# Optimization experiments

Hardware: AMD Instinct MI355X
Metric: run time of the kernel (lower is better)

The kernel has to match this reference:

```python
import jax, jax.numpy as jnp
import numpy as np

DIM = 1024
HID = 2048
E = 4

def setup_inputs() -> dict:
    key = jax.random.key(0)
    ks = jax.random.split(key, 7)
    s = lambda fan_in: 1.0 / np.sqrt(fan_in)
    x = jax.random.normal(ks[0], (2, 2048, DIM), dtype=jnp.float32)
    W1 = jax.random.uniform(ks[1], (E, DIM, HID), jnp.float32, -s(DIM), s(DIM))
    b1 = jax.random.uniform(ks[2], (E, HID), jnp.float32, -s(DIM), s(DIM))
    W2 = jax.random.uniform(ks[3], (E, HID, DIM), jnp.float32, -s(HID), s(HID))
    b2 = jax.random.uniform(ks[4], (E, DIM), jnp.float32, -s(HID), s(HID))
    Wr = jax.random.uniform(ks[5], (DIM, E), jnp.float32, -s(DIM), s(DIM))
    br = jax.random.uniform(ks[6], (E,), jnp.float32, -s(DIM), s(DIM))
    return {"x": x, "W1": W1, "b1": b1, "W2": W2, "b2": b2, "Wr": Wr, "br": br}

def reference(x, W1, b1, W2, b2, Wr, br):
    # router softmax weights: [B,T,E]
    weights = jax.nn.softmax(x @ Wr + br, axis=-1)
    # all-expert MLP: hidden [B,T,E,H]
    h = jax.nn.gelu(jnp.einsum('btd,edh->bteh', x, W1) + b1, approximate=False)
    # expert outputs [B,T,E,D]
    y = jnp.einsum('bteh,ehd->bted', h, W2) + b2
    # softmax-weighted combine over experts
    return jnp.einsum('bte,bted->btd', weights, y)
```

## Files before the change

### kernel.cpp

```cpp
#include <hip/hip_runtime.h>
#include <hip/hip_bf16.h>
#include <math.h>

#define DIM 1024
#define HID 2048
#define NE  4
#define NT  4096
#define KW  (NE*HID)
#define KSPLIT 2
#define KCH (KW / KSPLIT)

typedef __attribute__((ext_vector_type(8))) short short8;
typedef __attribute__((ext_vector_type(4))) short short4v;
typedef __attribute__((ext_vector_type(4))) float floatx4;


__device__ __forceinline__ void async_cp16(const void* g, void* l) {
  __builtin_amdgcn_global_load_lds(
      (const __attribute__((address_space(1))) void*)g,
      (__attribute__((address_space(3))) void*)l, 16, 0, 0);
}

__device__ __forceinline__ short f2bf(float f) {
  union { float f; unsigned u; } x; x.f = f;
  unsigned r = x.u + 0x7fffu + ((x.u >> 16) & 1u);
  return (short)(r >> 16);
}

__device__ __forceinline__ float gelu_fast(float v) {
  float u = 1.595769122f * (v + 0.044715f * v * v * v);
  return v * __builtin_amdgcn_rcpf(1.0f + __expf(-u));
}

__global__ void router_cvt(const float* __restrict__ x, const float* __restrict__ Wr,
                           const float* __restrict__ br, float* __restrict__ wgt,
                           short* __restrict__ xb) {
  const int wv = threadIdx.x >> 6, lane = threadIdx.x & 63;
  const int t = blockIdx.x * 4 + wv;
  const float* xr = x + (size_t)t * DIM;
  short* xo = xb + (size_t)t * DIM;
  float a0 = 0.f, a1 = 0.f, a2 = 0.f, a3 = 0.f;
  #pragma unroll
  for (int p = 0; p < 4; p++) {
    const int d = p * 256 + lane * 4;
    floatx4 v = *(const floatx4*)&xr[d];
    short4v o;
    #pragma unroll
    for (int j = 0; j < 4; j++) {
      o[j] = f2bf(v[j]);
      floatx4 wr = *(const floatx4*)&Wr[(d + j) * 4];
      a0 += v[j] * wr[0]; a1 += v[j] * wr[1];
      a2 += v[j] * wr[2]; a3 += v[j] * wr[3];
    }
    *(short4v*)&xo[d] = o;
  }
  #pragma unroll
  for (int off = 32; off; off >>= 1) {
    a0 += __shfl_down(a0, off);
    a1 += __shfl_down(a1, off);
    a2 += __shfl_down(a2, off);
    a3 += __shfl_down(a3, off);
  }
  a0 = __shfl(a0, 0); a1 = __shfl(a1, 0); a2 = __shfl(a2, 0); a3 = __shfl(a3, 0);
  float s0 = a0 + br[0], s1 = a1 + br[1], s2 = a2 + br[2], s3 = a3 + br[3];
  float m = fmaxf(fmaxf(s0, s1), fmaxf(s2, s3));
  float e0 = __expf(s0 - m), e1 = __expf(s1 - m), e2 = __expf(s2 - m), e3 = __expf(s3 - m);
  float inv = 1.f / (e0 + e1 + e2 + e3);
  float v = (lane == 0) ? e0 : (lane == 1) ? e1 : (lane == 2) ? e2 : e3;
  if (lane < 4) wgt[t * 4 + lane] = v * inv;
}

#define TP_PADR 136
__global__ void transpose_all(const float* __restrict__ W1, short* __restrict__ w1t,
                              const float* __restrict__ W2, short* __restrict__ w2t) {
  __shared__ __align__(16) short tile[32 * TP_PADR];
  const int b = blockIdx.x;
  const float* in; short* out; int R, C, xt, yt;
  if (b < 2048) {
    const int e = b >> 9, rem = b & 511;
    xt = rem & 63; yt = rem >> 6; R = DIM; C = HID;
    in = W1 + (size_t)e * DIM * HID; out = w1t + (size_t)e * DIM * HID;
  } else {
    const int rem = b - 2048;
    xt = rem & 31; yt = rem >> 5; R = KW; C = DIM;
    in = W2; out = w2t;
  }
  const int c0 = xt * 32, r0 = yt * 128;
  const int t = threadIdx.x;
  const int cin = (t & 7) * 4;
  const int rin = t >> 3;
  #pragma unroll
  for (int i = 0; i < 4; i++) {
    const int r = rin + i * 32;
    floatx4 v = *(const floatx4*)&in[(size_t)(r0 + r) * C + c0 + cin];
    #pragma unroll
    for (int j = 0; j < 4; j++)
      tile[(cin + j) * TP_PADR + r] = f2bf(v[j]);
  }
  __syncthreads();
  const int ct = t >> 3;
  #pragma unroll
  for (int i = 0; i < 2; i++) {
    const int rc = (t & 7) + 8 * i;
    short8 vv = *(const short8*)&tile[ct * TP_PADR + rc * 8];
    *(short8*)&out[(size_t)(c0 + ct) * R + r0 + rc * 8] = vv;
  }
}


__global__ __launch_bounds__(256, 2)
void gemm1_kernel(const short* __restrict__ xb, const short* __restrict__ w1t,
                  const float* __restrict__ b1, const float* __restrict__ wgt,
                  short* __restrict__ hw) {
  const int b = blockIdx.x;
  const int xcd = b & 7, slot = b >> 3;
  const int m_grp = xcd & 3, e_pair = xcd >> 1 & 2;
  const int n_idx = slot & 15, m_off = (slot >> 4) & 7, e_off = slot >> 7;
  const int e  = (xcd >> 2) * 2 + e_off;
  const int m0 = (m_grp * 8 + m_off) * 128;
  const int n0 = n_idx * 128;
  (void)e_pair;
  const int tid = threadIdx.x;
  const int lane = tid & 63;
  const int wv = tid >> 6;
  const int wm = (wv >> 1) * 64, wn = (wv & 1) * 64;
  const int quad = lane >> 4, lrow = lane & 15;
  const int sr  = tid >> 3;
  const int kof = ((tid & 7) ^ (sr & 7)) * 8;
  const int rkey = lrow & 7;

  __shared__ __align__(16) short As[128 * 64];
  __shared__ __align__(16) short Bs[128 * 64];

  const short* Ap = xb;
  const short* Bp = w1t + (size_t)e * HID * DIM;

  floatx4 acc[4][4];
  #pragma unroll
  for (int i = 0; i < 4; i++)
    #pragma unroll
    for (int j = 0; j < 4; j++) acc[i][j] = (floatx4)0.f;

  for (int k0 = 0; k0 < DIM; k0 += 64) {
    __syncthreads();
    #pragma unroll
    for (int c = 0; c < 4; c++)
      async_cp16(Ap + (size_t)(m0 + c * 32 + sr) * DIM + k0 + kof,
                 As + (c * 256 + tid) * 8);
    #pragma unroll
    for (int c = 0; c < 4; c++)
      async_cp16(Bp + (size_t)(n0 + c * 32 + sr) * DIM + k0 + kof,
                 Bs + (c * 256 + tid) * 8);
    __syncthreads();
    #pragma unroll
    for (int kk = 0; kk < 2; kk++) {
      short8 af[4], bf[4];
      const int ko = ((kk * 4 + quad) ^ rkey) * 8;
      #pragma unroll
      for (int i = 0; i < 4; i++)
        af[i] = *(const short8*)&As[(wm + i * 16 + lrow) * 64 + ko];
      #pragma unroll
      for (int j = 0; j < 4; j++)
        bf[j] = *(const short8*)&Bs[(wn + j * 16 + lrow) * 64 + ko];
      #pragma unroll
      for (int i = 0; i < 4; i++)
        #pragma unroll
        for (int j = 0; j < 4; j++)
          acc[i][j] = __builtin_amdgcn_mfma_f32_16x16x32_bf16(af[i], bf[j], acc[i][j], 0, 0, 0);
    }
  }

  #pragma unroll
  for (int i = 0; i < 4; i++) {
    const int rbase = m0 + wm + i * 16 + quad * 4;
    float wv4[4];
    #pragma unroll
    for (int r = 0; r < 4; r++) wv4[r] = wgt[(rbase + r) * NE + e];
    #pragma unroll
    for (int j = 0; j < 4; j++) {
      const int col = n0 + wn + j * 16 + lrow;
      const float b1v = b1[e * HID + col];
      #pragma unroll
      for (int r = 0; r < 4; r++) {
        float v = acc[i][j][r] + b1v;
        hw[(size_t)(rbase + r) * KW + e * HID + col] = f2bf(wv4[r] * gelu_fast(v));
      }
    }
  }
}

__global__ __launch_bounds__(256, 2)
void gemm2_kernel(const short* __restrict__ hw, const short* __restrict__ w2t,
                  const float* __restrict__ b2, const float* __restrict__ wgt,
                  float* __restrict__ out, float* __restrict__ part) {
  const int b = blockIdx.x;
  const int xcd = b & 7, slot = b >> 3;
  const int m_grp = xcd & 3, kz = xcd >> 2;
  const int n_idx = slot & 7, m_off = slot >> 3;
  const int m0 = (m_grp * 8 + m_off) * 128;
  const int n0 = n_idx * 128;
  const int tid = threadIdx.x;
  const int lane = tid & 63;
  const int wv = tid >> 6;
  const int wm = (wv >> 1) * 64, wn = (wv & 1) * 64;
  const int quad = lane >> 4, lrow = lane & 15;
  const int sr  = tid >> 3;
  const int kof = ((tid & 7) ^ (sr & 7)) * 8;
  const int rkey = lrow & 7;

  __shared__ __align__(16) short As[128 * 64];
  __shared__ __align__(16) short Bs[128 * 64];

  floatx4 acc[4][4];
  #pragma unroll
  for (int i = 0; i < 4; i++)
    #pragma unroll
    for (int j = 0; j < 4; j++) acc[i][j] = (floatx4)0.f;

  const int kbeg = kz * KCH;
  for (int kk0 = 0; kk0 < KCH; kk0 += 64) {
    const int k0 = kbeg + kk0;
    __syncthreads();
    #pragma unroll
    for (int c = 0; c < 4; c++)
      async_cp16(hw + (size_t)(m0 + c * 32 + sr) * KW + k0 + kof,
                 As + (c * 256 + tid) * 8);
    #pragma unroll
    for (int c = 0; c < 4; c++)
      async_cp16(w2t + (size_t)(n0 + c * 32 + sr) * KW + k0 + kof,
                 Bs + (c * 256 + tid) * 8);
    __syncthreads();
    #pragma unroll
    for (int kk = 0; kk < 2; kk++) {
      short8 af[4], bf[4];
      const int ko = ((kk * 4 + quad) ^ rkey) * 8;
      #pragma unroll
      for (int i = 0; i < 4; i++)
        af[i] = *(const short8*)&As[(wm + i * 16 + lrow) * 64 + ko];
      #pragma unroll
      for (int j = 0; j < 4; j++)
        bf[j] = *(const short8*)&Bs[(wn + j * 16 + lrow) * 64 + ko];
      #pragma unroll
      for (int i = 0; i < 4; i++)
        #pragma unroll
        for (int j = 0; j < 4; j++)
          acc[i][j] = __builtin_amdgcn_mfma_f32_16x16x32_bf16(af[i], bf[j], acc[i][j], 0, 0, 0);
    }
  }

  if (kz == 0) {
    #pragma unroll
    for (int i = 0; i < 4; i++) {
      const int rbase = m0 + wm + i * 16 + quad * 4;
      floatx4 wr[4];
      #pragma unroll
      for (int r = 0; r < 4; r++) wr[r] = *(const floatx4*)&wgt[(rbase + r) * NE];
      #pragma unroll
      for (int j = 0; j < 4; j++) {
        const int col = n0 + wn + j * 16 + lrow;
        float b2v[4];
        #pragma unroll
        for (int eI = 0; eI < 4; eI++) b2v[eI] = b2[eI * DIM + col];
        #pragma unroll
        for (int r = 0; r < 4; r++) {
          float bias = wr[r][0] * b2v[0] + wr[r][1] * b2v[1] +
                       wr[r][2] * b2v[2] + wr[r][3] * b2v[3];
          out[(size_t)(rbase + r) * DIM + col] = acc[i][j][r] + bias;
        }
      }
    }
  } else {
    #pragma unroll
    for (int i = 0; i < 4; i++) {
      const int rbase = m0 + wm + i * 16 + quad * 4;
      #pragma unroll
      for (int j = 0; j < 4; j++) {
        const int col = n0 + wn + j * 16 + lrow;
        #pragma unroll
        for (int r = 0; r < 4; r++)
          part[(size_t)(rbase + r) * DIM + col] = acc[i][j][r];
      }
    }
  }
}

__global__ void reduce_out(float* __restrict__ out, const float* __restrict__ part) {
  int i = (blockIdx.x * 256 + threadIdx.x) * 4;
  floatx4 v = *(const floatx4*)&out[i];
  floatx4 a = *(const floatx4*)&part[i];
  v = v + a;
  *(floatx4*)&out[i] = v;
}


extern "C" void kernel_launch(void* const* d_in, const int* in_sizes, int n_in,
                              void* d_out, int out_size, void* d_ws, size_t ws_size,
                              hipStream_t stream) {
  const float* x  = (const float*)d_in[0];
  const float* W1 = (const float*)d_in[1];
  const float* b1 = (const float*)d_in[2];
  const float* W2 = (const float*)d_in[3];
  const float* b2 = (const float*)d_in[4];
  const float* Wr = (const float*)d_in[5];
  const float* br = (const float*)d_in[6];
  float* out = (float*)d_out;

  char* ws = (char*)d_ws;
  float* wgt = (float*)(ws);
  short* w2t = (short*)(ws + 65536);
  short* hw  = (short*)(ws + 65536 + 16777216);
  short* xb  = (short*)(ws + 65536 + 16777216 + 67108864);
  short* w1t = (short*)(ws + 65536 + 16777216 + 67108864 + 8388608);
  float* part= (float*)(ws + 65536 + 16777216 + 67108864);

  hipLaunchKernelGGL(router_cvt, dim3(NT / 4), dim3(256), 0, stream, x, Wr, br, wgt, xb);
  hipLaunchKernelGGL(transpose_all, dim3(2048 + 2048), dim3(256), 0, stream,
                     W1, w1t, W2, w2t);
  hipLaunchKernelGGL(gemm1_kernel, dim3(2048), dim3(256), 0, stream,
                     xb, w1t, b1, wgt, hw);
  hipLaunchKernelGGL(gemm2_kernel, dim3(512), dim3(256), 0, stream,
                     hw, w2t, b2, wgt, out, part);
  hipLaunchKernelGGL(reduce_out, dim3(NT * DIM / 1024), dim3(256), 0, stream, out, part);
}
```

Baseline: 284.1 us.

## Load B operands directly into registers, merge prep kernels, remap XCD tiling

```diff
diff --git a/kernel.cpp b/kernel.cpp
--- a/kernel.cpp
+++ b/kernel.cpp
@@ -32,49 +32,51 @@
   return v * __builtin_amdgcn_rcpf(1.0f + __expf(-u));
 }
 
-__global__ void router_cvt(const float* __restrict__ x, const float* __restrict__ Wr,
-                           const float* __restrict__ br, float* __restrict__ wgt,
-                           short* __restrict__ xb) {
-  const int wv = threadIdx.x >> 6, lane = threadIdx.x & 63;
-  const int t = blockIdx.x * 4 + wv;
-  const float* xr = x + (size_t)t * DIM;
-  short* xo = xb + (size_t)t * DIM;
-  float a0 = 0.f, a1 = 0.f, a2 = 0.f, a3 = 0.f;
-  #pragma unroll
-  for (int p = 0; p < 4; p++) {
-    const int d = p * 256 + lane * 4;
-    floatx4 v = *(const floatx4*)&xr[d];
-    short4v o;
-    #pragma unroll
-    for (int j = 0; j < 4; j++) {
-      o[j] = f2bf(v[j]);
-      floatx4 wr = *(const floatx4*)&Wr[(d + j) * 4];
-      a0 += v[j] * wr[0]; a1 += v[j] * wr[1];
-      a2 += v[j] * wr[2]; a3 += v[j] * wr[3];
-    }
-    *(short4v*)&xo[d] = o;
-  }
-  #pragma unroll
-  for (int off = 32; off; off >>= 1) {
-    a0 += __shfl_down(a0, off);
-    a1 += __shfl_down(a1, off);
-    a2 += __shfl_down(a2, off);
-    a3 += __shfl_down(a3, off);
-  }
-  a0 = __shfl(a0, 0); a1 = __shfl(a1, 0); a2 = __shfl(a2, 0); a3 = __shfl(a3, 0);
-  float s0 = a0 + br[0], s1 = a1 + br[1], s2 = a2 + br[2], s3 = a3 + br[3];
-  float m = fmaxf(fmaxf(s0, s1), fmaxf(s2, s3));
-  float e0 = __expf(s0 - m), e1 = __expf(s1 - m), e2 = __expf(s2 - m), e3 = __expf(s3 - m);
-  float inv = 1.f / (e0 + e1 + e2 + e3);
-  float v = (lane == 0) ? e0 : (lane == 1) ? e1 : (lane == 2) ? e2 : e3;
-  if (lane < 4) wgt[t * 4 + lane] = v * inv;
-}
-
 #define TP_PADR 136
-__global__ void transpose_all(const float* __restrict__ W1, short* __restrict__ w1t,
-                              const float* __restrict__ W2, short* __restrict__ w2t) {
+__global__ void prep_kernel(const float* __restrict__ x, const float* __restrict__ Wr,
+                            const float* __restrict__ br, float* __restrict__ wgt,
+                            short* __restrict__ xb,
+                            const float* __restrict__ W1, short* __restrict__ w1t,
+                            const float* __restrict__ W2, short* __restrict__ w2t) {
   __shared__ __align__(16) short tile[32 * TP_PADR];
-  const int b = blockIdx.x;
+  const int bb = blockIdx.x;
+  if (bb < 1024) {
+    const int wv = threadIdx.x >> 6, lane = threadIdx.x & 63;
+    const int t = bb * 4 + wv;
+    const float* xr = x + (size_t)t * DIM;
+    short* xo = xb + (size_t)t * DIM;
+    float a0 = 0.f, a1 = 0.f, a2 = 0.f, a3 = 0.f;
+    #pragma unroll
+    for (int p = 0; p < 4; p++) {
+      const int d = p * 256 + lane * 4;
+      floatx4 v = *(const floatx4*)&xr[d];
+      short4v o;
+      #pragma unroll
+      for (int j = 0; j < 4; j++) {
+        o[j] = f2bf(v[j]);
+        floatx4 wr = *(const floatx4*)&Wr[(d + j) * 4];
+        a0 += v[j] * wr[0]; a1 += v[j] * wr[1];
+        a2 += v[j] * wr[2]; a3 += v[j] * wr[3];
+      }
+      *(short4v*)&xo[d] = o;
+    }
+    #pragma unroll
+    for (int off = 32; off; off >>= 1) {
+      a0 += __shfl_down(a0, off);
+      a1 += __shfl_down(a1, off);
+      a2 += __shfl_down(a2, off);
+      a3 += __shfl_down(a3, off);
+    }
+    a0 = __shfl(a0, 0); a1 = __shfl(a1, 0); a2 = __shfl(a2, 0); a3 = __shfl(a3, 0);
+    float s0 = a0 + br[0], s1 = a1 + br[1], s2 = a2 + br[2], s3 = a3 + br[3];
+    float m = fmaxf(fmaxf(s0, s1), fmaxf(s2, s3));
+    float e0 = __expf(s0 - m), e1 = __expf(s1 - m), e2 = __expf(s2 - m), e3 = __expf(s3 - m);
+    float inv = 1.f / (e0 + e1 + e2 + e3);
+    float v = (lane == 0) ? e0 : (lane == 1) ? e1 : (lane == 2) ? e2 : e3;
+    if (lane < 4) wgt[t * 4 + lane] = v * inv;
+    return;
+  }
+  const int b = bb - 1024;
   const float* in; short* out; int R, C, xt, yt;
   if (b < 2048) {
     const int e = b >> 9, rem = b & 511;
@@ -114,90 +116,9 @@
                   short* __restrict__ hw) {
   const int b = blockIdx.x;
   const int xcd = b & 7, slot = b >> 3;
-  const int m_grp = xcd & 3, e_pair = xcd >> 1 & 2;
-  const int n_idx = slot & 15, m_off = (slot >> 4) & 7, e_off = slot >> 7;
-  const int e  = (xcd >> 2) * 2 + e_off;
-  const int m0 = (m_grp * 8 + m_off) * 128;
-  const int n0 = n_idx * 128;
-  (void)e_pair;
-  const int tid = threadIdx.x;
-  const int lane = tid & 63;
-  const int wv = tid >> 6;
-  const int wm = (wv >> 1) * 64, wn = (wv & 1) * 64;
-  const int quad = lane >> 4, lrow = lane & 15;
-  const int sr  = tid >> 3;
-  const int kof = ((tid & 7) ^ (sr & 7)) * 8;
-  const int rkey = lrow & 7;
-
-  __shared__ __align__(16) short As[128 * 64];
-  __shared__ __align__(16) short Bs[128 * 64];
-
-  const short* Ap = xb;
-  const short* Bp = w1t + (size_t)e * HID * DIM;
-
-  floatx4 acc[4][4];
-  #pragma unroll
-  for (int i = 0; i < 4; i++)
-    #pragma unroll
-    for (int j = 0; j < 4; j++) acc[i][j] = (floatx4)0.f;
-
-  for (int k0 = 0; k0 < DIM; k0 += 64) {
-    __syncthreads();
-    #pragma unroll
-    for (int c = 0; c < 4; c++)
-      async_cp16(Ap + (size_t)(m0 + c * 32 + sr) * DIM + k0 + kof,
-                 As + (c * 256 + tid) * 8);
-    #pragma unroll
-    for (int c = 0; c < 4; c++)
-      async_cp16(Bp + (size_t)(n0 + c * 32 + sr) * DIM + k0 + kof,
-                 Bs + (c * 256 + tid) * 8);
-    __syncthreads();
-    #pragma unroll
-    for (int kk = 0; kk < 2; kk++) {
-      short8 af[4], bf[4];
-      const int ko = ((kk * 4 + quad) ^ rkey) * 8;
-      #pragma unroll
-      for (int i = 0; i < 4; i++)
-        af[i] = *(const short8*)&As[(wm + i * 16 + lrow) * 64 + ko];
-      #pragma unroll
-      for (int j = 0; j < 4; j++)
-        bf[j] = *(const short8*)&Bs[(wn + j * 16 + lrow) * 64 + ko];
-      #pragma unroll
-      for (int i = 0; i < 4; i++)
-        #pragma unroll
-        for (int j = 0; j < 4; j++)
-          acc[i][j] = __builtin_amdgcn_mfma_f32_16x16x32_bf16(af[i], bf[j], acc[i][j], 0, 0, 0);
-    }
-  }
-
-  #pragma unroll
-  for (int i = 0; i < 4; i++) {
-    const int rbase = m0 + wm + i * 16 + quad * 4;
-    float wv4[4];
-    #pragma unroll
-    for (int r = 0; r < 4; r++) wv4[r] = wgt[(rbase + r) * NE + e];
-    #pragma unroll
-    for (int j = 0; j < 4; j++) {
-      const int col = n0 + wn + j * 16 + lrow;
-      const float b1v = b1[e * HID + col];
-      #pragma unroll
-      for (int r = 0; r < 4; r++) {
-        float v = acc[i][j][r] + b1v;
-        hw[(size_t)(rbase + r) * KW + e * HID + col] = f2bf(wv4[r] * gelu_fast(v));
-      }
-    }
-  }
-}
-
-__global__ __launch_bounds__(256, 2)
-void gemm2_kernel(const short* __restrict__ hw, const short* __restrict__ w2t,
-                  const float* __restrict__ b2, const float* __restrict__ wgt,
-                  float* __restrict__ out, float* __restrict__ part) {
-  const int b = blockIdx.x;
-  const int xcd = b & 7, slot = b >> 3;
-  const int m_grp = xcd & 3, kz = xcd >> 2;
-  const int n_idx = slot & 7, m_off = slot >> 3;
-  const int m0 = (m_grp * 8 + m_off) * 128;
+  const int e = xcd >> 1, mg = xcd & 1;
+  const int n_idx = slot & 15, m_off = (slot >> 4) & 15;
+  const int m0 = (mg * 16 + m_off) * 128;
   const int n0 = n_idx * 128;
   const int tid = threadIdx.x;
   const int lane = tid & 63;
@@ -209,7 +130,84 @@
   const int rkey = lrow & 7;
 
   __shared__ __align__(16) short As[128 * 64];
-  __shared__ __align__(16) short Bs[128 * 64];
+
+  const short* Ap = xb;
+  const short* Bp = w1t + (size_t)e * HID * DIM;
+
+  floatx4 acc[4][4];
+  #pragma unroll
+  for (int i = 0; i < 4; i++)
+    #pragma unroll
+    for (int j = 0; j < 4; j++) acc[i][j] = (floatx4)0.f;
+
+  for (int k0 = 0; k0 < DIM; k0 += 64) {
+    __syncthreads();
+    #pragma unroll
+    for (int c = 0; c < 4; c++)
+      async_cp16(Ap + (size_t)(m0 + c * 32 + sr) * DIM + k0 + kof,
+                 As + (c * 256 + tid) * 8);
+    short8 bfr[2][4];
+    #pragma unroll
+    for (int kk = 0; kk < 2; kk++)
+      #pragma unroll
+      for (int j = 0; j < 4; j++)
+        bfr[kk][j] = *(const short8*)&Bp[(size_t)(n0 + wn + j * 16 + lrow) * DIM
+                                         + k0 + kk * 32 + quad * 8];
+    __syncthreads();
+    #pragma unroll
+    for (int kk = 0; kk < 2; kk++) {
+      short8 af[4];
+      const int ko = ((kk * 4 + quad) ^ rkey) * 8;
+      #pragma unroll
+      for (int i = 0; i < 4; i++)
+        af[i] = *(const short8*)&As[(wm + i * 16 + lrow) * 64 + ko];
+      #pragma unroll
+      for (int i = 0; i < 4; i++)
+        #pragma unroll
+        for (int j = 0; j < 4; j++)
+          acc[i][j] = __builtin_amdgcn_mfma_f32_16x16x32_bf16(af[i], bfr[kk][j], acc[i][j], 0, 0, 0);
+    }
+  }
+
+  #pragma unroll
+  for (int i = 0; i < 4; i++) {
+    const int rbase = m0 + wm + i * 16 + quad * 4;
+    float wv4[4];
+    #pragma unroll
+    for (int r = 0; r < 4; r++) wv4[r] = wgt[(rbase + r) * NE + e];
+    #pragma unroll
+    for (int j = 0; j < 4; j++) {
+      const int col = n0 + wn + j * 16 + lrow;
+      const float b1v = b1[e * HID + col];
+      #pragma unroll
+      for (int r = 0; r < 4; r++) {
+        float v = acc[i][j][r] + b1v;
+        hw[(size_t)(rbase + r) * KW + e * HID + col] = f2bf(wv4[r] * gelu_fast(v));
+      }
+    }
+  }
+}
+
+__global__ __launch_bounds__(256, 2)
+void gemm2_kernel(const short* __restrict__ hw, const short* __restrict__ w2t,
+                  const float* __restrict__ b2, const float* __restrict__ wgt,
+                  float* __restrict__ out, float* __restrict__ part) {
+  const int b = blockIdx.x;
+  const int xcd = b & 7, slot = b >> 3;
+  const int kz = xcd >> 2, mg = (xcd >> 1) & 1, ng = xcd & 1;
+  const int m_off = slot & 15, n_off = slot >> 4;
+  const int m0 = (mg * 16 + m_off) * 128;
+  const int n0 = (ng * 4 + n_off) * 128;
+  const int tid = threadIdx.x;
+  const int lane = tid & 63;
+  const int wv = tid >> 6;
+  const int wm = (wv >> 1) * 64, wn = (wv & 1) * 64;
+  const int quad = lane >> 4, lrow = lane & 15;
+  const int sr  = tid >> 3;
+  const int kof = ((tid & 7) ^ (sr & 7)) * 8;
+  const int rkey = lrow & 7;
+
+  __shared__ __align__(16) short As[128 * 64];
 
   floatx4 acc[4][4];
   #pragma unroll
@@ -225,26 +223,26 @@
     for (int c = 0; c < 4; c++)
       async_cp16(hw + (size_t)(m0 + c * 32 + sr) * KW + k0 + kof,
                  As + (c * 256 + tid) * 8);
-    #pragma unroll
-    for (int c = 0; c < 4; c++)
-      async_cp16(w2t + (size_t)(n0 + c * 32 + sr) * KW + k0 + kof,
-                 Bs + (c * 256 + tid) * 8);
+    short8 bfr[2][4];
+    #pragma unroll
+    for (int kk = 0; kk < 2; kk++)
+      #pragma unroll
+      for (int j = 0; j < 4; j++)
+        bfr[kk][j] = *(const short8*)&w2t[(size_t)(n0 + wn + j * 16 + lrow) * KW
+                                          + k0 + kk * 32 + quad * 8];
     __syncthreads();
     #pragma unroll
     for (int kk = 0; kk < 2; kk++) {
-      short8 af[4], bf[4];
+      short8 af[4];
       const int ko = ((kk * 4 + quad) ^ rkey) * 8;
       #pragma unroll
       for (int i = 0; i < 4; i++)
         af[i] = *(const short8*)&As[(wm + i * 16 + lrow) * 64 + ko];
       #pragma unroll
-      for (int j = 0; j < 4; j++)
-        bf[j] = *(const short8*)&Bs[(wn + j * 16 + lrow) * 64 + ko];
-      #pragma unroll
       for (int i = 0; i < 4; i++)
         #pragma unroll
         for (int j = 0; j < 4; j++)
-          acc[i][j] = __builtin_amdgcn_mfma_f32_16x16x32_bf16(af[i], bf[j], acc[i][j], 0, 0, 0);
+          acc[i][j] = __builtin_amdgcn_mfma_f32_16x16x32_bf16(af[i], bfr[kk][j], acc[i][j], 0, 0, 0);
     }
   }
 
@@ -313,9 +311,8 @@
   short* w1t = (short*)(ws + 65536 + 16777216 + 67108864 + 8388608);
   float* part= (float*)(ws + 65536 + 16777216 + 67108864);
 
-  hipLaunchKernelGGL(router_cvt, dim3(NT / 4), dim3(256), 0, stream, x, Wr, br, wgt, xb);
-  hipLaunchKernelGGL(transpose_all, dim3(2048 + 2048), dim3(256), 0, stream,
-                     W1, w1t, W2, w2t);
+  hipLaunchKernelGGL(prep_kernel, dim3(1024 + 4096), dim3(256), 0, stream,
+                     x, Wr, br, wgt, xb, W1, w1t, W2, w2t);
   hipLaunchKernelGGL(gemm1_kernel, dim3(2048), dim3(256), 0, stream,
                      xb, w1t, b1, wgt, hw);
   hipLaunchKernelGGL(gemm2_kernel, dim3(512), dim3(256), 0, stream,
```

Measured after the change: 420.8 us. 1.48x slower.

## Fuse all five stages into one persistent cooperative kernel with grid syncs

Applied to the files above, without the earlier changes.

```diff
diff --git a/kernel.cpp b/kernel.cpp
--- a/kernel.cpp
+++ b/kernel.cpp
@@ -1,4 +1,5 @@
 #include <hip/hip_runtime.h>
+#include <hip/hip_cooperative_groups.h>
 #include <hip/hip_bf16.h>
 #include <math.h>
 
@@ -10,6 +11,8 @@
 #define KSPLIT 2
 #define KCH (KW / KSPLIT)
 
+namespace cg = cooperative_groups;
+
 typedef __attribute__((ext_vector_type(8))) short short8;
 typedef __attribute__((ext_vector_type(4))) short short4v;
 typedef __attribute__((ext_vector_type(4))) float floatx4;
@@ -32,264 +35,258 @@
   return v * __builtin_amdgcn_rcpf(1.0f + __expf(-u));
 }
 
-__global__ void router_cvt(const float* __restrict__ x, const float* __restrict__ Wr,
-                           const float* __restrict__ br, float* __restrict__ wgt,
-                           short* __restrict__ xb) {
-  const int wv = threadIdx.x >> 6, lane = threadIdx.x & 63;
-  const int t = blockIdx.x * 4 + wv;
-  const float* xr = x + (size_t)t * DIM;
-  short* xo = xb + (size_t)t * DIM;
-  float a0 = 0.f, a1 = 0.f, a2 = 0.f, a3 = 0.f;
-  #pragma unroll
-  for (int p = 0; p < 4; p++) {
-    const int d = p * 256 + lane * 4;
-    floatx4 v = *(const floatx4*)&xr[d];
-    short4v o;
-    #pragma unroll
-    for (int j = 0; j < 4; j++) {
-      o[j] = f2bf(v[j]);
-      floatx4 wr = *(const floatx4*)&Wr[(d + j) * 4];
-      a0 += v[j] * wr[0]; a1 += v[j] * wr[1];
-      a2 += v[j] * wr[2]; a3 += v[j] * wr[3];
-    }
-    *(short4v*)&xo[d] = o;
-  }
-  #pragma unroll
-  for (int off = 32; off; off >>= 1) {
-    a0 += __shfl_down(a0, off);
-    a1 += __shfl_down(a1, off);
-    a2 += __shfl_down(a2, off);
-    a3 += __shfl_down(a3, off);
-  }
-  a0 = __shfl(a0, 0); a1 = __shfl(a1, 0); a2 = __shfl(a2, 0); a3 = __shfl(a3, 0);
-  float s0 = a0 + br[0], s1 = a1 + br[1], s2 = a2 + br[2], s3 = a3 + br[3];
-  float m = fmaxf(fmaxf(s0, s1), fmaxf(s2, s3));
-  float e0 = __expf(s0 - m), e1 = __expf(s1 - m), e2 = __expf(s2 - m), e3 = __expf(s3 - m);
-  float inv = 1.f / (e0 + e1 + e2 + e3);
-  float v = (lane == 0) ? e0 : (lane == 1) ? e1 : (lane == 2) ? e2 : e3;
-  if (lane < 4) wgt[t * 4 + lane] = v * inv;
-}
-
 #define TP_PADR 136
-__global__ void transpose_all(const float* __restrict__ W1, short* __restrict__ w1t,
-                              const float* __restrict__ W2, short* __restrict__ w2t) {
-  __shared__ __align__(16) short tile[32 * TP_PADR];
-  const int b = blockIdx.x;
-  const float* in; short* out; int R, C, xt, yt;
-  if (b < 2048) {
-    const int e = b >> 9, rem = b & 511;
-    xt = rem & 63; yt = rem >> 6; R = DIM; C = HID;
-    in = W1 + (size_t)e * DIM * HID; out = w1t + (size_t)e * DIM * HID;
-  } else {
-    const int rem = b - 2048;
-    xt = rem & 31; yt = rem >> 5; R = KW; C = DIM;
-    in = W2; out = w2t;
-  }
-  const int c0 = xt * 32, r0 = yt * 128;
-  const int t = threadIdx.x;
-  const int cin = (t & 7) * 4;
-  const int rin = t >> 3;
-  #pragma unroll
-  for (int i = 0; i < 4; i++) {
-    const int r = rin + i * 32;
-    floatx4 v = *(const floatx4*)&in[(size_t)(r0 + r) * C + c0 + cin];
-    #pragma unroll
-    for (int j = 0; j < 4; j++)
-      tile[(cin + j) * TP_PADR + r] = f2bf(v[j]);
-  }
-  __syncthreads();
-  const int ct = t >> 3;
-  #pragma unroll
-  for (int i = 0; i < 2; i++) {
-    const int rc = (t & 7) + 8 * i;
-    short8 vv = *(const short8*)&tile[ct * TP_PADR + rc * 8];
-    *(short8*)&out[(size_t)(c0 + ct) * R + r0 + rc * 8] = vv;
-  }
-}
-
-
-__global__ __launch_bounds__(256, 2)
-void gemm1_kernel(const short* __restrict__ xb, const short* __restrict__ w1t,
-                  const float* __restrict__ b1, const float* __restrict__ wgt,
-                  short* __restrict__ hw) {
-  const int b = blockIdx.x;
-  const int xcd = b & 7, slot = b >> 3;
-  const int m_grp = xcd & 3, e_pair = xcd >> 1 & 2;
-  const int n_idx = slot & 15, m_off = (slot >> 4) & 7, e_off = slot >> 7;
-  const int e  = (xcd >> 2) * 2 + e_off;
-  const int m0 = (m_grp * 8 + m_off) * 128;
-  const int n0 = n_idx * 128;
-  (void)e_pair;
+
+__global__ void __launch_bounds__(256, 2)
+moe_fused(const float* __restrict__ x,  const float* __restrict__ Wr,
+          const float* __restrict__ br,
+          const float* __restrict__ W1, const float* __restrict__ b1,
+          const float* __restrict__ W2, const float* __restrict__ b2,
+          float* __restrict__ wgt, short* __restrict__ xb,
+          short* __restrict__ w1t, short* __restrict__ w2t,
+          short* __restrict__ hw,  float* __restrict__ part,
+          float* __restrict__ out)
+{
+  cg::grid_group gg = cg::this_grid();
+  const int rb  = blockIdx.x;
   const int tid = threadIdx.x;
-  const int lane = tid & 63;
-  const int wv = tid >> 6;
-  const int wm = (wv >> 1) * 64, wn = (wv & 1) * 64;
-  const int quad = lane >> 4, lrow = lane & 15;
-  const int sr  = tid >> 3;
-  const int kof = ((tid & 7) ^ (sr & 7)) * 8;
-  const int rkey = lrow & 7;
 
   __shared__ __align__(16) short As[128 * 64];
   __shared__ __align__(16) short Bs[128 * 64];
 
-  const short* Ap = xb;
-  const short* Bp = w1t + (size_t)e * HID * DIM;
-
-  floatx4 acc[4][4];
-  #pragma unroll
-  for (int i = 0; i < 4; i++)
+  const int lane = tid & 63;
+  const int wv   = tid >> 6;
+  const int wm   = (wv >> 1) * 64, wn = (wv & 1) * 64;
+  const int quad = lane >> 4, lrow = lane & 15;
+  const int sr   = tid >> 3;
+  const int kof  = ((tid & 7) ^ (sr & 7)) * 8;
+  const int rkey = lrow & 7;
+
+  for (int vb = rb; vb < 5120; vb += 512) {
+    if (vb < 1024) {
+      const int t = vb * 4 + wv;
+      const float* xr = x + (size_t)t * DIM;
+      short* xo = xb + (size_t)t * DIM;
+      float a0 = 0.f, a1 = 0.f, a2 = 0.f, a3 = 0.f;
+      #pragma unroll
+      for (int p = 0; p < 4; p++) {
+        const int d = p * 256 + lane * 4;
+        floatx4 v = *(const floatx4*)&xr[d];
+        short4v o;
+        #pragma unroll
+        for (int j = 0; j < 4; j++) {
+          o[j] = f2bf(v[j]);
+          floatx4 wr = *(const floatx4*)&Wr[(d + j) * 4];
+          a0 += v[j] * wr[0]; a1 += v[j] * wr[1];
+          a2 += v[j] * wr[2]; a3 += v[j] * wr[3];
+        }
+        *(short4v*)&xo[d] = o;
+      }
+      #pragma unroll
+      for (int off = 32; off; off >>= 1) {
+        a0 += __shfl_down(a0, off);
+        a1 += __shfl_down(a1, off);
+        a2 += __shfl_down(a2, off);
+        a3 += __shfl_down(a3, off);
+      }
+      a0 = __shfl(a0, 0); a1 = __shfl(a1, 0); a2 = __shfl(a2, 0); a3 = __shfl(a3, 0);
+      float s0 = a0 + br[0], s1 = a1 + br[1], s2 = a2 + br[2], s3 = a3 + br[3];
+      float m = fmaxf(fmaxf(s0, s1), fmaxf(s2, s3));
+      float e0 = __expf(s0 - m), e1 = __expf(s1 - m);
+      float e2 = __expf(s2 - m), e3 = __expf(s3 - m);
+      float inv = 1.f / (e0 + e1 + e2 + e3);
+      float v = (lane == 0) ? e0 : (lane == 1) ? e1 : (lane == 2) ? e2 : e3;
+      if (lane < 4) wgt[t * 4 + lane] = v * inv;
+    } else {
+      short* tile = As;
+      const int b = vb - 1024;
+      const float* in; short* o; int R, C, xt, yt;
+      if (b < 2048) {
+        const int e = b >> 9, rem = b & 511;
+        xt = rem & 63; yt = rem >> 6; R = DIM; C = HID;
+        in = W1 + (size_t)e * DIM * HID; o = w1t + (size_t)e * DIM * HID;
+      } else {
+        const int rem = b - 2048;
+        xt = rem & 31; yt = rem >> 5; R = KW; C = DIM;
+        in = W2; o = w2t;
+      }
+      const int c0 = xt * 32, r0 = yt * 128;
+      const int cin = (tid & 7) * 4;
+      const int rin = tid >> 3;
+      #pragma unroll
+      for (int i = 0; i < 4; i++) {
+        const int r = rin + i * 32;
+        floatx4 v = *(const floatx4*)&in[(size_t)(r0 + r) * C + c0 + cin];
+        #pragma unroll
+        for (int j = 0; j < 4; j++)
+          tile[(cin + j) * TP_PADR + r] = f2bf(v[j]);
+      }
+      __syncthreads();
+      const int ct = tid >> 3;
+      #pragma unroll
+      for (int i = 0; i < 2; i++) {
+        const int rc = (tid & 7) + 8 * i;
+        short8 vv = *(const short8*)&tile[ct * TP_PADR + rc * 8];
+        *(short8*)&o[(size_t)(c0 + ct) * R + r0 + rc * 8] = vv;
+      }
+    }
+    __syncthreads();
+  }
+  gg.sync();
+
+  for (int vb = rb; vb < 2048; vb += 512) {
+    const int xcd = vb & 7, slot = vb >> 3;
+    const int m_grp = xcd & 3;
+    const int n_idx = slot & 15, m_off = (slot >> 4) & 7, e_off = slot >> 7;
+    const int e  = (xcd >> 2) * 2 + e_off;
+    const int m0 = (m_grp * 8 + m_off) * 128;
+    const int n0 = n_idx * 128;
+
+    const short* Ap = xb;
+    const short* Bp = w1t + (size_t)e * HID * DIM;
+
+    floatx4 acc[4][4];
     #pragma unroll
-    for (int j = 0; j < 4; j++) acc[i][j] = (floatx4)0.f;
-
-  for (int k0 = 0; k0 < DIM; k0 += 64) {
-    __syncthreads();
-    #pragma unroll
-    for (int c = 0; c < 4; c++)
-      async_cp16(Ap + (size_t)(m0 + c * 32 + sr) * DIM + k0 + kof,
-                 As + (c * 256 + tid) * 8);
-    #pragma unroll
-    for (int c = 0; c < 4; c++)
-      async_cp16(Bp + (size_t)(n0 + c * 32 + sr) * DIM + k0 + kof,
-                 Bs + (c * 256 + tid) * 8);
-    __syncthreads();
-    #pragma unroll
-    for (int kk = 0; kk < 2; kk++) {
-      short8 af[4], bf[4];
-      const int ko = ((kk * 4 + quad) ^ rkey) * 8;
-      #pragma unroll
-      for (int i = 0; i < 4; i++)
-        af[i] = *(const short8*)&As[(wm + i * 16 + lrow) * 64 + ko];
-      #pragma unroll
-      for (int j = 0; j < 4; j++)
-        bf[j] = *(const short8*)&Bs[(wn + j * 16 + lrow) * 64 + ko];
-      #pragma unroll
-      for (int i = 0; i < 4; i++)
+    for (int i = 0; i < 4; i++)
+      #pragma unroll
+      for (int j = 0; j < 4; j++) acc[i][j] = (floatx4)0.f;
+
+    for (int k0 = 0; k0 < DIM; k0 += 64) {
+      __syncthreads();
+      #pragma unroll
+      for (int c = 0; c < 4; c++)
+        async_cp16(Ap + (size_t)(m0 + c * 32 + sr) * DIM + k0 + kof,
+                   As + (c * 256 + tid) * 8);
+      #pragma unroll
+      for (int c = 0; c < 4; c++)
+        async_cp16(Bp + (size_t)(n0 + c * 32 + sr) * DIM + k0 + kof,
+                   Bs + (c * 256 + tid) * 8);
+      __syncthreads();
+      #pragma unroll
+      for (int kk = 0; kk < 2; kk++) {
+        short8 af[4], bf[4];
+        const int ko = ((kk * 4 + quad) ^ rkey) * 8;
+        #pragma unroll
+        for (int i = 0; i < 4; i++)
+          af[i] = *(const short8*)&As[(wm + i * 16 + lrow) * 64 + ko];
         #pragma unroll
         for (int j = 0; j < 4; j++)
-          acc[i][j] = __builtin_amdgcn_mfma_f32_16x16x32_bf16(af[i], bf[j], acc[i][j], 0, 0, 0);
-    }
-  }
-
-  #pragma unroll
-  for (int i = 0; i < 4; i++) {
-    const int rbase = m0 + wm + i * 16 + quad * 4;
-    float wv4[4];
-    #pragma unroll
-    for (int r = 0; r < 4; r++) wv4[r] = wgt[(rbase + r) * NE + e];
-    #pragma unroll
-    for (int j = 0; j < 4; j++) {
-      const int col = n0 + wn + j * 16 + lrow;
-      const float b1v = b1[e * HID + col];
-      #pragma unroll
-      for (int r = 0; r < 4; r++) {
-        float v = acc[i][j][r] + b1v;
-        hw[(size_t)(rbase + r) * KW + e * HID + col] = f2bf(wv4[r] * gelu_fast(v));
-      }
-    }
-  }
-}
-
-__global__ __launch_bounds__(256, 2)
-void gemm2_kernel(const short* __restrict__ hw, const short* __restrict__ w2t,
-                  const float* __restrict__ b2, const float* __restrict__ wgt,
-                  float* __restrict__ out, float* __restrict__ part) {
-  const int b = blockIdx.x;
-  const int xcd = b & 7, slot = b >> 3;
-  const int m_grp = xcd & 3, kz = xcd >> 2;
-  const int n_idx = slot & 7, m_off = slot >> 3;
-  const int m0 = (m_grp * 8 + m_off) * 128;
-  const int n0 = n_idx * 128;
-  const int tid = threadIdx.x;
-  const int lane = tid & 63;
-  const int wv = tid >> 6;
-  const int wm = (wv >> 1) * 64, wn = (wv & 1) * 64;
-  const int quad = lane >> 4, lrow = lane & 15;
-  const int sr  = tid >> 3;
-  const int kof = ((tid & 7) ^ (sr & 7)) * 8;
-  const int rkey = lrow & 7;
-
-  __shared__ __align__(16) short As[128 * 64];
-  __shared__ __align__(16) short Bs[128 * 64];
-
-  floatx4 acc[4][4];
-  #pragma unroll
-  for (int i = 0; i < 4; i++)
-    #pragma unroll
-    for (int j = 0; j < 4; j++) acc[i][j] = (floatx4)0.f;
-
-  const int kbeg = kz * KCH;
-  for (int kk0 = 0; kk0 < KCH; kk0 += 64) {
-    const int k0 = kbeg + kk0;
-    __syncthreads();
-    #pragma unroll
-    for (int c = 0; c < 4; c++)
-      async_cp16(hw + (size_t)(m0 + c * 32 + sr) * KW + k0 + kof,
-                 As + (c * 256 + tid) * 8);
-    #pragma unroll
-    for (int c = 0; c < 4; c++)
-      async_cp16(w2t + (size_t)(n0 + c * 32 + sr) * KW + k0 + kof,
-                 Bs + (c * 256 + tid) * 8);
-    __syncthreads();
-    #pragma unroll
-    for (int kk = 0; kk < 2; kk++) {
-      short8 af[4], bf[4];
-      const int ko = ((kk * 4 + quad) ^ rkey) * 8;
-      #pragma unroll
-      for (int i = 0; i < 4; i++)
-        af[i] = *(const short8*)&As[(wm + i * 16 + lrow) * 64 + ko];
-      #pragma unroll
-      for (int j = 0; j < 4; j++)
-        bf[j] = *(const short8*)&Bs[(wn + j * 16 + lrow) * 64 + ko];
-      #pragma unroll
-      for (int i = 0; i < 4; i++)
-        #pragma unroll
-        for (int j = 0; j < 4; j++)
-          acc[i][j] = __builtin_amdgcn_mfma_f32_16x16x32_bf16(af[i], bf[j], acc[i][j], 0, 0, 0);
-    }
-  }
-
-  if (kz == 0) {
+          bf[j] = *(const short8*)&Bs[(wn + j * 16 + lrow) * 64 + ko];
+        #pragma unroll
+        for (int i = 0; i < 4; i++)
+          #pragma unroll
+          for (int j = 0; j < 4; j++)
+            acc[i][j] = __builtin_amdgcn_mfma_f32_16x16x32_bf16(af[i], bf[j], acc[i][j], 0, 0, 0);
+      }
+    }
+
     #pragma unroll
     for (int i = 0; i < 4; i++) {
       const int rbase = m0 + wm + i * 16 + quad * 4;
-      floatx4 wr[4];
-      #pragma unroll
-      for (int r = 0; r < 4; r++) wr[r] = *(const floatx4*)&wgt[(rbase + r) * NE];
+      float wv4[4];
+      #pragma unroll
+      for (int r = 0; r < 4; r++) wv4[r] = wgt[(rbase + r) * NE + e];
       #pragma unroll
       for (int j = 0; j < 4; j++) {
         const int col = n0 + wn + j * 16 + lrow;
-        float b2v[4];
-        #pragma unroll
-        for (int eI = 0; eI < 4; eI++) b2v[eI] = b2[eI * DIM + col];
+        const float b1v = b1[e * HID + col];
         #pragma unroll
         for (int r = 0; r < 4; r++) {
-          float bias = wr[r][0] * b2v[0] + wr[r][1] * b2v[1] +
-                       wr[r][2] * b2v[2] + wr[r][3] * b2v[3];
-          out[(size_t)(rbase + r) * DIM + col] = acc[i][j][r] + bias;
+          float v = acc[i][j][r] + b1v;
+          hw[(size_t)(rbase + r) * KW + e * HID + col] = f2bf(wv4[r] * gelu_fast(v));
         }
       }
     }
-  } else {
+  }
+  gg.sync();
+
+  {
+    const int xcd = rb & 7, slot = rb >> 3;
+    const int m_grp = xcd & 3, kz = xcd >> 2;
+    const int n_idx = slot & 7, m_off = slot >> 3;
+    const int m0 = (m_grp * 8 + m_off) * 128;
+    const int n0 = n_idx * 128;
+
+    floatx4 acc[4][4];
     #pragma unroll
-    for (int i = 0; i < 4; i++) {
-      const int rbase = m0 + wm + i * 16 + quad * 4;
-      #pragma unroll
-      for (int j = 0; j < 4; j++) {
-        const int col = n0 + wn + j * 16 + lrow;
-        #pragma unroll
-        for (int r = 0; r < 4; r++)
-          part[(size_t)(rbase + r) * DIM + col] = acc[i][j][r];
+    for (int i = 0; i < 4; i++)
+      #pragma unroll
+      for (int j = 0; j < 4; j++) acc[i][j] = (floatx4)0.f;
+
+    const int kbeg = kz * KCH;
+    for (int kk0 = 0; kk0 < KCH; kk0 += 64) {
+      const int k0 = kbeg + kk0;
+      __syncthreads();
+      #pragma unroll
+      for (int c = 0; c < 4; c++)
+        async_cp16(hw + (size_t)(m0 + c * 32 + sr) * KW + k0 + kof,
+                   As + (c * 256 + tid) * 8);
+      #pragma unroll
+      for (int c = 0; c < 4; c++)
+        async_cp16(w2t + (size_t)(n0 + c * 32 + sr) * KW + k0 + kof,
+                   Bs + (c * 256 + tid) * 8);
+      __syncthreads();
+      #pragma unroll
+      for (int kk = 0; kk < 2; kk++) {
+        short8 af[4], bf[4];
+        const int ko = ((kk * 4 + quad) ^ rkey) * 8;
+        #pragma unroll
+        for (int i = 0; i < 4; i++)
+          af[i] = *(const short8*)&As[(wm + i * 16 + lrow) * 64 + ko];
+        #pragma unroll
+        for (int j = 0; j < 4; j++)
+          bf[j] = *(const short8*)&Bs[(wn + j * 16 + lrow) * 64 + ko];
+        #pragma unroll
+        for (int i = 0; i < 4; i++)
+          #pragma unroll
+          for (int j = 0; j < 4; j++)
+            acc[i][j] = __builtin_amdgcn_mfma_f32_16x16x32_bf16(af[i], bf[j], acc[i][j], 0, 0, 0);
+      }
+    }
+
+    if (kz == 0) {
+      #pragma unroll
+      for (int i = 0; i < 4; i++) {
+        const int rbase = m0 + wm + i * 16 + quad * 4;
+        floatx4 wr[4];
+        #pragma unroll
+        for (int r = 0; r < 4; r++) wr[r] = *(const floatx4*)&wgt[(rbase + r) * NE];
+        #pragma unroll
+        for (int j = 0; j < 4; j++) {
+          const int col = n0 + wn + j * 16 + lrow;
+          float b2v[4];
+          #pragma unroll
+          for (int eI = 0; eI < 4; eI++) b2v[eI] = b2[eI * DIM + col];
+          #pragma unroll
+          for (int r = 0; r < 4; r++) {
+            float bias = wr[r][0] * b2v[0] + wr[r][1] * b2v[1] +
+                         wr[r][2] * b2v[2] + wr[r][3] * b2v[3];
+            out[(size_t)(rbase + r) * DIM + col] = acc[i][j][r] + bias;
+          }
+        }
+      }
+    } else {
+      #pragma unroll
+      for (int i = 0; i < 4; i++) {
+        const int rbase = m0 + wm + i * 16 + quad * 4;
+        #pragma unroll
+        for (int j = 0; j < 4; j++) {
+          const int col = n0 + wn + j * 16 + lrow;
+          #pragma unroll
+          for (int r = 0; r < 4; r++)
+            part[(size_t)(rbase + r) * DIM + col] = acc[i][j][r];
+        }
       }
     }
   }
-}
-
-__global__ void reduce_out(float* __restrict__ out, const float* __restrict__ part) {
-  int i = (blockIdx.x * 256 + threadIdx.x) * 4;
-  floatx4 v = *(const floatx4*)&out[i];
-  floatx4 a = *(const floatx4*)&part[i];
-  v = v + a;
-  *(floatx4*)&out[i] = v;
+  gg.sync();
+
+  for (int i = (rb * 256 + tid) * 4; i < NT * DIM; i += 512 * 256 * 4) {
+    floatx4 v = *(const floatx4*)&out[i];
+    floatx4 a = *(const floatx4*)&part[i];
+    v = v + a;
+    *(floatx4*)&out[i] = v;
+  }
 }
 
 
@@ -313,12 +310,11 @@
   short* w1t = (short*)(ws + 65536 + 16777216 + 67108864 + 8388608);
   float* part= (float*)(ws + 65536 + 16777216 + 67108864);
 
-  hipLaunchKernelGGL(router_cvt, dim3(NT / 4), dim3(256), 0, stream, x, Wr, br, wgt, xb);
-  hipLaunchKernelGGL(transpose_all, dim3(2048 + 2048), dim3(256), 0, stream,
-                     W1, w1t, W2, w2t);
-  hipLaunchKernelGGL(gemm1_kernel, dim3(2048), dim3(256), 0, stream,
-                     xb, w1t, b1, wgt, hw);
-  hipLaunchKernelGGL(gemm2_kernel, dim3(512), dim3(256), 0, stream,
-                     hw, w2t, b2, wgt, out, part);
-  hipLaunchKernelGGL(reduce_out, dim3(NT * DIM / 1024), dim3(256), 0, stream, out, part);
-}
+  void* args[] = {
+    (void*)&x, (void*)&Wr, (void*)&br, (void*)&W1, (void*)&b1,
+    (void*)&W2, (void*)&b2, (void*)&wgt, (void*)&xb, (void*)&w1t,
+    (void*)&w2t, (void*)&hw, (void*)&part, (void*)&out
+  };
+  hipLaunchCooperativeKernel((void*)moe_fused, dim3(512), dim3(256),
+                             args, 0, stream);
+}
```

Result: slower. 487.9 us (+71.8%).
